# Kernel tuning notes

Hardware: AMD Instinct MI355X
Metric: run time of the kernel (lower is better)

Reference implementation:

```python
import jax, jax.numpy as jnp
import numpy as np

N = 50000      # nodes
E = 800000     # edges
IN = 128       # in_channels
HID = 32       # hidden_channels per head
HEADS = 4
OUT = 16       # out_channels
NEG_SLOPE_ATT = 0.2   # GATv2Conv default negative_slope
NEG_SLOPE_ACT = 0.01  # F.leaky_relu default
EPS = 1e-16


def setup_inputs() -> dict:
    key = jax.random.key(0)
    ks = jax.random.split(key, 13)
    d1 = HEADS * HID  # 128
    g = lambda k, shape, fan: jax.random.normal(k, shape, jnp.float32) * (1.0 / np.sqrt(fan))
    return {
        "x": jax.random.normal(ks[0], (N, IN), jnp.float32),
        "edge_index": jax.random.randint(ks[1], (2, E), 0, N, dtype=jnp.int32),
        "edge_weight": jax.random.uniform(ks[2], (E,), jnp.float32),
        # conv1 (GATv2): lin_l, lin_r, att, bias
        "Wl1": g(ks[3], (IN, d1), IN), "Wr1": g(ks[4], (IN, d1), IN),
        "att1": g(ks[5], (HEADS, HID), HID), "b1": jnp.zeros((d1,), jnp.float32),
        # conv2
        "Wl2": g(ks[6], (d1, d1), d1), "Wr2": g(ks[7], (d1, d1), d1),
        "att2": g(ks[8], (HEADS, HID), HID), "b2": jnp.zeros((d1,), jnp.float32),
        # classifier
        "Wc": g(ks[9], (d1, OUT), d1), "bc": jnp.zeros((OUT,), jnp.float32),
    }


def gatv2_layer(x, Wl, Wr, att, bias, src, dst):
    n = x.shape[0]
    xl = (x @ Wl).reshape(n, HEADS, HID)  # source transform
    xr = (x @ Wr).reshape(n, HEADS, HID)  # target transform
    m = xl[src] + xr[dst]                                    # [Etot, H, C]
    e = jnp.sum(jax.nn.leaky_relu(m, NEG_SLOPE_ATT) * att, axis=-1)  # [Etot, H]
    # segment softmax over incoming edges of each target node
    emax = jax.ops.segment_max(e, dst, num_segments=n)       # [N, H]
    ex = jnp.exp(e - emax[dst])
    denom = jax.ops.segment_sum(ex, dst, num_segments=n)     # [N, H]
    alpha = ex / (denom[dst] + EPS)                          # [Etot, H]
    out = jax.ops.segment_sum(xl[src] * alpha[:, :, None], dst, num_segments=n)  # [N, H, C]
    return out.reshape(n, HEADS * HID) + bias


def reference(x, edge_index, edge_weight, Wl1, Wr1, att1, b1, Wl2, Wr2, att2, b2, Wc, bc):
    # GATv2Conv default add_self_loops=True
    loops = jnp.arange(N, dtype=edge_index.dtype)
    src = jnp.concatenate([edge_index[0], loops])
    dst = jnp.concatenate([edge_index[1], loops])
    h = gatv2_layer(x, Wl1, Wr1, att1, b1, src, dst)
    h = jax.nn.leaky_relu(h, NEG_SLOPE_ACT)
    h = gatv2_layer(h, Wl2, Wr2, att2, b2, src, dst)
    h = jax.nn.leaky_relu(h, NEG_SLOPE_ACT)
    logits = h @ Wc + bc
    return (logits, h)
```

## Files before the change

### kernel.cpp

```cpp
#include <hip/hip_runtime.h>
#include <hip/hip_fp16.h>


#define LOG2E 1.4426950408889634f
#define AST 40

typedef short bf16x8 __attribute__((ext_vector_type(8)));
typedef float f32x4 __attribute__((ext_vector_type(4)));

__device__ __forceinline__ unsigned short f2bf(float f) {
  union { float f; unsigned u; } x; x.f = f;
  unsigned r = x.u + 0x7fffu + ((x.u >> 16) & 1u);
  return (unsigned short)(r >> 16);
}
__device__ __forceinline__ float bf2f(unsigned short h) {
  union { unsigned u; float f; } x; x.u = ((unsigned)h) << 16;
  return x.f;
}
__device__ __forceinline__ void split4(float4 v, ushort4& h, ushort4& l) {
  h.x = f2bf(v.x); l.x = f2bf(v.x - bf2f(h.x));
  h.y = f2bf(v.y); l.y = f2bf(v.y - bf2f(h.y));
  h.z = f2bf(v.z); l.z = f2bf(v.z - bf2f(h.z));
  h.w = f2bf(v.w); l.w = f2bf(v.w - bf2f(h.w));
}


__global__ __launch_bounds__(256) void zero_i32(int* __restrict__ p, int n) {
  int i = blockIdx.x * 256 + threadIdx.x;
  if (i < n) p[i] = 0;
}

__global__ __launch_bounds__(256) void count_kernel(const int* __restrict__ dst,
                                                    int* __restrict__ cnt, int E) {
  int i = blockIdx.x * 256 + threadIdx.x;
  if (i < E) atomicAdd(&cnt[dst[i]], 1);
}

__global__ __launch_bounds__(256) void scan_blk(const int* __restrict__ cnt,
                                                int* __restrict__ excl,
                                                int* __restrict__ bsum, int n) {
  __shared__ int s[256];
  int t = threadIdx.x, i = blockIdx.x * 256 + t;
  int v = (i < n) ? (cnt[i] + 1) : 0;
  s[t] = v;
  __syncthreads();
#pragma unroll
  for (int off = 1; off < 256; off <<= 1) {
    int u = (t >= off) ? s[t - off] : 0;
    __syncthreads();
    s[t] += u;
    __syncthreads();
  }
  if (i < n) excl[i] = s[t] - v;
  if (t == 255) bsum[blockIdx.x] = s[255];
}

__global__ __launch_bounds__(256) void scan_bsum(int* __restrict__ bsum, int nb,
                                                 int* __restrict__ row_start, int n) {
  __shared__ int s[256];
  int t = threadIdx.x;
  int v = (t < nb) ? bsum[t] : 0;
  s[t] = v;
  __syncthreads();
#pragma unroll
  for (int off = 1; off < 256; off <<= 1) {
    int u = (t >= off) ? s[t - off] : 0;
    __syncthreads();
    s[t] += u;
    __syncthreads();
  }
  if (t < nb) bsum[t] = s[t] - v;
  if (t == 255) row_start[n] = s[255];
}

__global__ __launch_bounds__(256) void scan_add(int* __restrict__ row_start,
                                                const int* __restrict__ bsum,
                                                int* __restrict__ wpos,
                                                int* __restrict__ csr,
                                                int n, int padBase) {
  int i = blockIdx.x * 256 + threadIdx.x;
  if (i < n) {
    int r = row_start[i] + bsum[blockIdx.x];
    row_start[i] = r;
    wpos[i] = r + 1;
    csr[r] = i;
  }
  if (blockIdx.x == 0 && threadIdx.x < 16) csr[padBase + threadIdx.x] = 0;
}

__global__ __launch_bounds__(256) void scatter_kernel(const int* __restrict__ src,
                                                      const int* __restrict__ dst,
                                                      int* __restrict__ wpos,
                                                      int* __restrict__ csr,
                                                      int E, int sliceSize) {
  int slice = blockIdx.x & 7;
  int chunk = blockIdx.x >> 3;
  int nchunk = gridDim.x >> 3;
  int lo = slice * sliceSize, hi = lo + sliceSize;
  int per = (E + nchunk - 1) / nchunk;
  int b = chunk * per;
  int e = min(b + per, E);
  for (int i = b + threadIdx.x; i < e; i += 256) {
    int d = dst[i];
    if (d >= lo && d < hi) {
      int p = atomicAdd(&wpos[d], 1);
      csr[p] = src[i];
    }
  }
}

__global__ __launch_bounds__(256) void convert_W(const float* __restrict__ Wl1,
                                                 const float* __restrict__ Wr1,
                                                 const float* __restrict__ Wl2,
                                                 const float* __restrict__ Wr2,
                                                 unsigned short* __restrict__ BT1h,
                                                 unsigned short* __restrict__ BT1l,
                                                 unsigned short* __restrict__ BT2h,
                                                 unsigned short* __restrict__ BT2l) {
  int b = blockIdx.x;
  const float* Wl = (b < 128) ? Wl1 : Wl2;
  const float* Wr = (b < 128) ? Wr1 : Wr2;
  unsigned short* BTh = (b < 128) ? BT1h : BT2h;
  unsigned short* BTl = (b < 128) ? BT1l : BT2l;
  int idx = (b & 127) * 256 + threadIdx.x;
  int col = idx >> 7, k = idx & 127;
  float v = (col < 128) ? Wl[k * 128 + col] : Wr[k * 128 + (col - 128)];
  unsigned short h = f2bf(v);
  BTh[idx] = h;
  BTl[idx] = f2bf(v - bf2f(h));
}

enum { IN_F32 = 0, IN_F16 = 1 };
template <int MODE>
__global__ __launch_bounds__(256) void gemm_mfma(
    const float* __restrict__ Af, const __half* __restrict__ Af16,
    const unsigned short* __restrict__ BTh, const unsigned short* __restrict__ BTl,
    __half* __restrict__ Cl, __half* __restrict__ Cr, int nrows) {
  __shared__ unsigned short sAh[128 * AST], sAl[128 * AST];
  __shared__ unsigned short sBh[128 * AST], sBl[128 * AST];
  int tid = threadIdx.x;
  int wave = tid >> 6, lane = tid & 63;
  int rowBase = blockIdx.x * 128;
  int colBase = blockIdx.y * 128;
  int rowHalf = (wave >> 1) * 64;
  int colHalf = (wave & 1) * 64;
  int l15 = lane & 15, quad = lane >> 4;

  f32x4 acc[4][4];
#pragma unroll
  for (int m = 0; m < 4; ++m)
#pragma unroll
    for (int n = 0; n < 4; ++n) acc[m][n] = (f32x4){0.f, 0.f, 0.f, 0.f};

  for (int kc = 0; kc < 4; ++kc) {
#pragma unroll
    for (int i = 0; i < 2; ++i) {
      int idx = tid + i * 256;
      int row = idx >> 2, seg = idx & 3;
      int gr = rowBase + row;
      if (MODE == IN_F32) {
        float4 v0 = make_float4(0.f, 0.f, 0.f, 0.f), v1 = v0;
        if (gr < nrows) {
          v0 = *(const float4*)&Af[(size_t)gr * 128 + kc * 32 + seg * 8];
          v1 = *(const float4*)&Af[(size_t)gr * 128 + kc * 32 + seg * 8 + 4];
        }
        ushort4 h0, l0, h1, l1;
        split4(v0, h0, l0);
        split4(v1, h1, l1);
        *(ushort4*)&sAh[row * AST + seg * 8] = h0;
        *(ushort4*)&sAh[row * AST + seg * 8 + 4] = h1;
        *(ushort4*)&sAl[row * AST + seg * 8] = l0;
        *(ushort4*)&sAl[row * AST + seg * 8 + 4] = l1;
      } else {
        uint4 raw = make_uint4(0, 0, 0, 0);
        if (gr < nrows)
          raw = *(const uint4*)&Af16[(size_t)gr * 128 + kc * 32 + seg * 8];
        const __half* hp = (const __half*)&raw;
        float4 v0 = make_float4(__half2float(hp[0]), __half2float(hp[1]),
                                __half2float(hp[2]), __half2float(hp[3]));
        float4 v1 = make_float4(__half2float(hp[4]), __half2float(hp[5]),
                                __half2float(hp[6]), __half2float(hp[7]));
        ushort4 h0, l0, h1, l1;
        split4(v0, h0, l0);
        split4(v1, h1, l1);
        *(ushort4*)&sAh[row * AST + seg * 8] = h0;
        *(ushort4*)&sAh[row * AST + seg * 8 + 4] = h1;
        *(ushort4*)&sAl[row * AST + seg * 8] = l0;
        *(ushort4*)&sAl[row * AST + seg * 8 + 4] = l1;
      }
    }
#pragma unroll
    for (int i = 0; i < 2; ++i) {
      int idx = tid + i * 256;
      int col = idx >> 2, seg = idx & 3;
      *(uint4*)&sBh[col * AST + seg * 8] =
          *(const uint4*)&BTh[(size_t)(colBase + col) * 128 + kc * 32 + seg * 8];
      *(uint4*)&sBl[col * AST + seg * 8] =
          *(const uint4*)&BTl[(size_t)(colBase + col) * 128 + kc * 32 + seg * 8];
    }
    __syncthreads();

    bf16x8 afh[4], afl[4], bfh[4], bfl[4];
#pragma unroll
    for (int m = 0; m < 4; ++m) {
      int r = rowHalf + m * 16 + l15;
      afh[m] = *(const bf16x8*)&sAh[r * AST + quad * 8];
      afl[m] = *(const bf16x8*)&sAl[r * AST + quad * 8];
    }
#pragma unroll
    for (int n = 0; n < 4; ++n) {
      int cc = colHalf + n * 16 + l15;
      bfh[n] = *(const bf16x8*)&sBh[cc * AST + quad * 8];
      bfl[n] = *(const bf16x8*)&sBl[cc * AST + quad * 8];
    }
#pragma unroll
    for (int m = 0; m < 4; ++m)
#pragma unroll
      for (int n = 0; n < 4; ++n) {
        acc[m][n] = __builtin_amdgcn_mfma_f32_16x16x32_bf16(afh[m], bfh[n], acc[m][n], 0, 0, 0);
        acc[m][n] = __builtin_amdgcn_mfma_f32_16x16x32_bf16(afh[m], bfl[n], acc[m][n], 0, 0, 0);
        acc[m][n] = __builtin_amdgcn_mfma_f32_16x16x32_bf16(afl[m], bfh[n], acc[m][n], 0, 0, 0);
      }
    __syncthreads();
  }

  __half* __restrict__ C = (blockIdx.y == 0) ? Cl : Cr;
#pragma unroll
  for (int m = 0; m < 4; ++m)
#pragma unroll
    for (int r = 0; r < 4; ++r) {
      int grow = rowBase + rowHalf + m * 16 + quad * 4 + r;
      if (grow < nrows) {
#pragma unroll
        for (int n = 0; n < 4; ++n)
          C[(size_t)grow * 128 + colHalf + n * 16 + l15] = __float2half(acc[m][n][r]);
      }
    }
}

__global__ __launch_bounds__(256) void gat_attn(const __half* __restrict__ xl,
                                                const __half* __restrict__ xr,
                                                const int* __restrict__ row_start,
                                                const int* __restrict__ csr,
                                                const float* __restrict__ att,
                                                const float* __restrict__ bias,
                                                float* __restrict__ ofp,
                                                __half* __restrict__ oh16,
                                                int n_nodes) {
  int node = blockIdx.x * 4 + (threadIdx.x >> 6);
  if (node >= n_nodes) return;
  int lane = threadIdx.x & 63;
  int slot = lane >> 4;
  int l15 = lane & 15;
  int c0 = l15 * 8;

  float fxr[8];
  {
    uint4 raw = *(const uint4*)&xr[(size_t)node * 128 + c0];
    const __half* hp = (const __half*)&raw;
#pragma unroll
    for (int k = 0; k < 8; ++k) fxr[k] = __half2float(hp[k]);
  }
  float a06[8], a04[8];
  {
    float4 a0 = *(const float4*)&att[c0];
    float4 a1 = *(const float4*)&att[c0 + 4];
    float av[8] = {a0.x, a0.y, a0.z, a0.w, a1.x, a1.y, a1.z, a1.w};
    const float C06 = 0.6f * LOG2E, C04 = 0.4f * LOG2E;
#pragma unroll
    for (int k = 0; k < 8; ++k) { a06[k] = av[k] * C06; a04[k] = av[k] * C04; }
  }

  float acc[8];
#pragma unroll
  for (int k = 0; k < 8; ++k) acc[k] = 0.f;
  float lsum = 0.f;

#define EDGE_BODY(SRC, PVALID)                                                 \
  {                                                                            \
    uint4 raw = *(const uint4*)&xl[(size_t)(unsigned)(SRC)*128 + c0];          \
    const __half* hp = (const __half*)&raw;                                    \
    float e = 0.f;                                                             \
    _Pragma("unroll") for (int k = 0; k < 8; ++k) {                            \
      float t = __half2float(hp[k]) + fxr[k];                                  \
      e = fmaf(a06[k], t, e);                                                  \
      e = fmaf(a04[k], fabsf(t), e);                                           \
    }                                                                          \
    e += __shfl_xor(e, 1);                                                     \
    e += __shfl_xor(e, 2);                                                     \
    float p = (PVALID) ? __builtin_amdgcn_exp2f(e) : 0.f;                      \
    lsum += p;                                                                 \
    _Pragma("unroll") for (int k = 0; k < 8; ++k)                              \
        acc[k] = fmaf(p, __half2float(hp[k]), acc[k]);                         \
  }

  int beg = row_start[node], end = row_start[node + 1];
  int deg = end - beg;
  int fullEnd = beg + (deg & ~15);

  for (int base = beg; base < fullEnd; base += 16) {
    int b0 = base + 4 * slot;
    int s0 = csr[b0], s1 = csr[b0 + 1], s2 = csr[b0 + 2], s3 = csr[b0 + 3];
    EDGE_BODY(s0, true);
    EDGE_BODY(s1, true);
    EDGE_BODY(s2, true);
    EDGE_BODY(s3, true);
  }
  for (int base = fullEnd; base < end; base += 4) {
    int idx = base + slot;
    int src = csr[idx];
    EDGE_BODY(src, idx < end);
  }
#undef EDGE_BODY

  lsum += __shfl_xor(lsum, 16);
  lsum += __shfl_xor(lsum, 32);
#pragma unroll
  for (int k = 0; k < 8; ++k) {
    acc[k] += __shfl_xor(acc[k], 16);
    acc[k] += __shfl_xor(acc[k], 32);
  }

  if (slot == 0) {
    float4 b0v = *(const float4*)&bias[c0];
    float4 b1v = *(const float4*)&bias[c0 + 4];
    float bv[8] = {b0v.x, b0v.y, b0v.z, b0v.w, b1v.x, b1v.y, b1v.z, b1v.w};
    float inv = 1.f / (lsum + 1e-16f);
    float o[8];
#pragma unroll
    for (int k = 0; k < 8; ++k) {
      float v = fmaf(acc[k], inv, bv[k]);
      o[k] = fmaf(0.495f, fabsf(v), 0.505f * v);
    }
    if (ofp) {
      *(float4*)&ofp[(size_t)node * 128 + c0] = make_float4(o[0], o[1], o[2], o[3]);
      *(float4*)&ofp[(size_t)node * 128 + c0 + 4] = make_float4(o[4], o[5], o[6], o[7]);
    }
    if (oh16) {
      ushort4 ha, hb;
      ha.x = __half_as_ushort(__float2half(o[0]));
      ha.y = __half_as_ushort(__float2half(o[1]));
      ha.z = __half_as_ushort(__float2half(o[2]));
      ha.w = __half_as_ushort(__float2half(o[3]));
      hb.x = __half_as_ushort(__float2half(o[4]));
      hb.y = __half_as_ushort(__float2half(o[5]));
      hb.z = __half_as_ushort(__float2half(o[6]));
      hb.w = __half_as_ushort(__float2half(o[7]));
      *(ushort4*)&oh16[(size_t)node * 128 + c0] = ha;
      *(ushort4*)&oh16[(size_t)node * 128 + c0 + 4] = hb;
    }
  }
}

__global__ __launch_bounds__(256) void classifier_kernel(const float4* __restrict__ h4,
                                                         const float* __restrict__ Wc,
                                                         const float* __restrict__ bc,
                                                         float* __restrict__ logits,
                                                         int n) {
  __shared__ float sW[2048];
  __shared__ float sb[16];
  int t = threadIdx.x;
#pragma unroll
  for (int i = 0; i < 8; ++i) sW[t + i * 256] = Wc[t + i * 256];
  if (t < 16) sb[t] = bc[t];
  __syncthreads();
  int node = blockIdx.x * 256 + t;
  if (node >= n) return;
  float acc[16];
#pragma unroll
  for (int o = 0; o < 16; ++o) acc[o] = sb[o];
  for (int c4 = 0; c4 < 32; ++c4) {
    float4 hv = h4[(unsigned)node * 32 + c4];
    const float* w = &sW[c4 * 64];
#pragma unroll
    for (int o = 0; o < 16; ++o) {
      acc[o] = fmaf(hv.x, w[o], acc[o]);
      acc[o] = fmaf(hv.y, w[16 + o], acc[o]);
      acc[o] = fmaf(hv.z, w[32 + o], acc[o]);
      acc[o] = fmaf(hv.w, w[48 + o], acc[o]);
    }
  }
#pragma unroll
  for (int q = 0; q < 4; ++q)
    *(float4*)&logits[(size_t)node * 16 + q * 4] =
        make_float4(acc[q * 4], acc[q * 4 + 1], acc[q * 4 + 2], acc[q * 4 + 3]);
}


extern "C" void kernel_launch(void* const* d_in, const int* in_sizes, int n_in,
                              void* d_out, int out_size, void* d_ws, size_t ws_size,
                              hipStream_t stream) {
  const float* x    = (const float*)d_in[0];
  const int*   ei   = (const int*)d_in[1];
  const float* Wl1  = (const float*)d_in[3];
  const float* Wr1  = (const float*)d_in[4];
  const float* att1 = (const float*)d_in[5];
  const float* b1   = (const float*)d_in[6];
  const float* Wl2  = (const float*)d_in[7];
  const float* Wr2  = (const float*)d_in[8];
  const float* att2 = (const float*)d_in[9];
  const float* b2   = (const float*)d_in[10];
  const float* Wc   = (const float*)d_in[11];
  const float* bc   = (const float*)d_in[12];

  const int N = in_sizes[0] / 128;
  const int E = in_sizes[1] / 2;

  float* outp   = (float*)d_out;
  float* logits = outp;
  float* hout   = outp + (size_t)N * 16;
  __half* h1f16 = (__half*)hout;

  char* ws = (char*)d_ws;
  __half* xlbuf = (__half*)ws;                ws += (size_t)N * 128 * 2;
  __half* xrbuf = (__half*)ws;                ws += (size_t)N * 128 * 2;
  unsigned short* WT1h = (unsigned short*)ws; ws += 256 * 128 * 2;
  unsigned short* WT1l = (unsigned short*)ws; ws += 256 * 128 * 2;
  unsigned short* WT2h = (unsigned short*)ws; ws += 256 * 128 * 2;
  unsigned short* WT2l = (unsigned short*)ws; ws += 256 * 128 * 2;
  int* cnt       = (int*)ws;                  ws += (size_t)N * 4;
  int* row_start = (int*)ws;                  ws += (size_t)(N + 1) * 4;
  int* wpos      = (int*)ws;                  ws += (size_t)N * 4;
  int* bsum      = (int*)ws;                  ws += 256 * 4;
  int* csr       = (int*)ws;                  ws += (size_t)(E + N + 16) * 4;

  const int* esrc = ei;
  const int* edst = ei + E;

  int gN = (N + 255) / 256, gE = (E + 255) / 256;
  dim3 gGemm((N + 127) / 128, 2);
  int gAttn = (N + 3) / 4;
  int sliceSize = (N + 7) / 8;

  zero_i32<<<gN, 256, 0, stream>>>(cnt, N);
  count_kernel<<<gE, 256, 0, stream>>>(edst, cnt, E);
  scan_blk<<<gN, 256, 0, stream>>>(cnt, row_start, bsum, N);
  scan_bsum<<<1, 256, 0, stream>>>(bsum, gN, row_start, N);
  scan_add<<<gN, 256, 0, stream>>>(row_start, bsum, wpos, csr, N, E + N);
  scatter_kernel<<<1024, 256, 0, stream>>>(esrc, edst, wpos, csr, E, sliceSize);

  convert_W<<<256, 256, 0, stream>>>(Wl1, Wr1, Wl2, Wr2, WT1h, WT1l, WT2h, WT2l);

  gemm_mfma<IN_F32><<<gGemm, 256, 0, stream>>>(x, nullptr, WT1h, WT1l,
                                               xlbuf, xrbuf, N);
  gat_attn<<<gAttn, 256, 0, stream>>>(xlbuf, xrbuf, row_start, csr, att1, b1,
                                      nullptr, h1f16, N);

  gemm_mfma<IN_F16><<<gGemm, 256, 0, stream>>>(nullptr, h1f16, WT2h, WT2l,
                                               xlbuf, xrbuf, N);
  gat_attn<<<gAttn, 256, 0, stream>>>(xlbuf, xrbuf, row_start, csr, att2, b2,
                                      hout, nullptr, N);

  classifier_kernel<<<(N + 255) / 256, 256, 0, stream>>>((const float4*)hout, Wc, bc,
                                                         logits, N);
}
```

Baseline: 323.3 us.

## Co-schedule CSR scatter with layer-1 GEMM and merge weight conversion into count

The weight conversion is folded into the edge-count kernel as extra blocks. The CSR scatter becomes part of the layer-1 GEMM launch: groups of nine blocks hold five scatter blocks and four GEMM tiles, so the atomic-bound scatter can overlap MFMA work. This removes two launches and their serialization. It also unrolls the scatter loop four times, reads esrc only for edges that fall in the block's slice, and raises wave priority around the MFMA section, at the cost of more complex block indexing and mixed resource usage in one grid.

```diff
diff --git a/kernel.cpp b/kernel.cpp
--- a/kernel.cpp
+++ b/kernel.cpp
@@ -28,12 +28,6 @@
 __global__ __launch_bounds__(256) void zero_i32(int* __restrict__ p, int n) {
   int i = blockIdx.x * 256 + threadIdx.x;
   if (i < n) p[i] = 0;
-}
-
-__global__ __launch_bounds__(256) void count_kernel(const int* __restrict__ dst,
-                                                    int* __restrict__ cnt, int E) {
-  int i = blockIdx.x * 256 + threadIdx.x;
-  if (i < E) atomicAdd(&cnt[dst[i]], 1);
 }
 
 __global__ __launch_bounds__(256) void scan_blk(const int* __restrict__ cnt,
@@ -88,36 +82,18 @@
   if (blockIdx.x == 0 && threadIdx.x < 16) csr[padBase + threadIdx.x] = 0;
 }
 
-__global__ __launch_bounds__(256) void scatter_kernel(const int* __restrict__ src,
-                                                      const int* __restrict__ dst,
-                                                      int* __restrict__ wpos,
-                                                      int* __restrict__ csr,
-                                                      int E, int sliceSize) {
-  int slice = blockIdx.x & 7;
-  int chunk = blockIdx.x >> 3;
-  int nchunk = gridDim.x >> 3;
-  int lo = slice * sliceSize, hi = lo + sliceSize;
-  int per = (E + nchunk - 1) / nchunk;
-  int b = chunk * per;
-  int e = min(b + per, E);
-  for (int i = b + threadIdx.x; i < e; i += 256) {
-    int d = dst[i];
-    if (d >= lo && d < hi) {
-      int p = atomicAdd(&wpos[d], 1);
-      csr[p] = src[i];
-    }
-  }
-}
-
-__global__ __launch_bounds__(256) void convert_W(const float* __restrict__ Wl1,
-                                                 const float* __restrict__ Wr1,
-                                                 const float* __restrict__ Wl2,
-                                                 const float* __restrict__ Wr2,
-                                                 unsigned short* __restrict__ BT1h,
-                                                 unsigned short* __restrict__ BT1l,
-                                                 unsigned short* __restrict__ BT2h,
-                                                 unsigned short* __restrict__ BT2l) {
+__global__ __launch_bounds__(256) void convert_count(
+    const float* __restrict__ Wl1, const float* __restrict__ Wr1,
+    const float* __restrict__ Wl2, const float* __restrict__ Wr2,
+    unsigned short* __restrict__ BT1h, unsigned short* __restrict__ BT1l,
+    unsigned short* __restrict__ BT2h, unsigned short* __restrict__ BT2l,
+    const int* __restrict__ dst, int* __restrict__ cnt, int E) {
   int b = blockIdx.x;
+  if (b >= 256) {
+    int i = (b - 256) * 256 + threadIdx.x;
+    if (i < E) atomicAdd(&cnt[dst[i]], 1);
+    return;
+  }
   const float* Wl = (b < 128) ? Wl1 : Wl2;
   const float* Wr = (b < 128) ? Wr1 : Wr2;
   unsigned short* BTh = (b < 128) ? BT1h : BT2h;
@@ -131,17 +107,84 @@
 }
 
 enum { IN_F32 = 0, IN_F16 = 1 };
-template <int MODE>
+#define NSCAT 1152
+#define NCHUNK 128
+template <int MODE, int FUSE>
 __global__ __launch_bounds__(256) void gemm_mfma(
     const float* __restrict__ Af, const __half* __restrict__ Af16,
     const unsigned short* __restrict__ BTh, const unsigned short* __restrict__ BTl,
-    __half* __restrict__ Cl, __half* __restrict__ Cr, int nrows) {
-  __shared__ unsigned short sAh[128 * AST], sAl[128 * AST];
-  __shared__ unsigned short sBh[128 * AST], sBl[128 * AST];
+    __half* __restrict__ Cl, __half* __restrict__ Cr, int nrows,
+    const int* __restrict__ esrc, const int* __restrict__ edst,
+    int* __restrict__ wpos, int* __restrict__ csr, int E, int sliceSize) {
+  __shared__ __align__(16) unsigned short smem[4 * 128 * AST];
   int tid = threadIdx.x;
+  int bx, by;
+  if (FUSE) {
+    int g = blockIdx.x / 9, r = blockIdx.x - g * 9;
+    if (r < 5) {
+      int sid = g * 5 + r;
+      if (sid < NSCAT) {
+        int slice = blockIdx.x & 7;
+        int chunk = (g >> 3) * 5;
+        for (int gp = g & ~7; gp < g; ++gp)
+          chunk += (((slice - gp) & 7) < 5) ? 1 : 0;
+        if (chunk < NCHUNK) {
+          int per = (E + NCHUNK - 1) / NCHUNK;
+          int b0 = chunk * per;
+          int ee = min(b0 + per, E);
+          int lo = slice * sliceSize, hi = lo + sliceSize;
+          int i = b0 + tid;
+          for (; i + 768 < ee; i += 1024) {
+            int d0 = edst[i];
+            int d1 = edst[i + 256];
+            int d2 = edst[i + 512];
+            int d3 = edst[i + 768];
+            if (d0 >= lo && d0 < hi) {
+              int s = esrc[i];
+              int p = atomicAdd(&wpos[d0], 1); csr[p] = s;
+            }
+            if (d1 >= lo && d1 < hi) {
+              int s = esrc[i + 256];
+              int p = atomicAdd(&wpos[d1], 1); csr[p] = s;
+            }
+            if (d2 >= lo && d2 < hi) {
+              int s = esrc[i + 512];
+              int p = atomicAdd(&wpos[d2], 1); csr[p] = s;
+            }
+            if (d3 >= lo && d3 < hi) {
+              int s = esrc[i + 768];
+              int p = atomicAdd(&wpos[d3], 1); csr[p] = s;
+            }
+          }
+          for (; i < ee; i += 256) {
+            int d = edst[i];
+            if (d >= lo && d < hi) {
+              int s = esrc[i];
+              int p = atomicAdd(&wpos[d], 1); csr[p] = s;
+            }
+          }
+        }
+      }
+      return;
+    }
+    int gid = g * 4 + (r - 5);
+    int nbx = (nrows + 127) >> 7;
+    if (gid >= nbx * 2) return;
+    bx = gid >> 1;
+    by = gid & 1;
+  } else {
+    bx = blockIdx.x;
+    by = blockIdx.y;
+  }
+
+  unsigned short* sAh = smem;
+  unsigned short* sAl = smem + 5120;
+  unsigned short* sBh = smem + 10240;
+  unsigned short* sBl = smem + 15360;
+
   int wave = tid >> 6, lane = tid & 63;
-  int rowBase = blockIdx.x * 128;
-  int colBase = blockIdx.y * 128;
+  int rowBase = bx * 128;
+  int colBase = by * 128;
   int rowHalf = (wave >> 1) * 64;
   int colHalf = (wave & 1) * 64;
   int l15 = lane & 15, quad = lane >> 4;
@@ -158,36 +201,29 @@
       int idx = tid + i * 256;
       int row = idx >> 2, seg = idx & 3;
       int gr = rowBase + row;
+      float4 v0 = make_float4(0.f, 0.f, 0.f, 0.f), v1 = v0;
       if (MODE == IN_F32) {
-        float4 v0 = make_float4(0.f, 0.f, 0.f, 0.f), v1 = v0;
         if (gr < nrows) {
           v0 = *(const float4*)&Af[(size_t)gr * 128 + kc * 32 + seg * 8];
           v1 = *(const float4*)&Af[(size_t)gr * 128 + kc * 32 + seg * 8 + 4];
         }
-        ushort4 h0, l0, h1, l1;
-        split4(v0, h0, l0);
-        split4(v1, h1, l1);
-        *(ushort4*)&sAh[row * AST + seg * 8] = h0;
-        *(ushort4*)&sAh[row * AST + seg * 8 + 4] = h1;
-        *(ushort4*)&sAl[row * AST + seg * 8] = l0;
-        *(ushort4*)&sAl[row * AST + seg * 8 + 4] = l1;
       } else {
-        uint4 raw = make_uint4(0, 0, 0, 0);
-        if (gr < nrows)
-          raw = *(const uint4*)&Af16[(size_t)gr * 128 + kc * 32 + seg * 8];
-        const __half* hp = (const __half*)&raw;
-        float4 v0 = make_float4(__half2float(hp[0]), __half2float(hp[1]),
-                                __half2float(hp[2]), __half2float(hp[3]));
-        float4 v1 = make_float4(__half2float(hp[4]), __half2float(hp[5]),
-                                __half2float(hp[6]), __half2float(hp[7]));
-        ushort4 h0, l0, h1, l1;
-        split4(v0, h0, l0);
-        split4(v1, h1, l1);
-        *(ushort4*)&sAh[row * AST + seg * 8] = h0;
-        *(ushort4*)&sAh[row * AST + seg * 8 + 4] = h1;
-        *(ushort4*)&sAl[row * AST + seg * 8] = l0;
-        *(ushort4*)&sAl[row * AST + seg * 8 + 4] = l1;
+        if (gr < nrows) {
+          uint4 raw = *(const uint4*)&Af16[(size_t)gr * 128 + kc * 32 + seg * 8];
+          const __half* hp = (const __half*)&raw;
+          v0 = make_float4(__half2float(hp[0]), __half2float(hp[1]),
+                           __half2float(hp[2]), __half2float(hp[3]));
+          v1 = make_float4(__half2float(hp[4]), __half2float(hp[5]),
+                           __half2float(hp[6]), __half2float(hp[7]));
+        }
       }
+      ushort4 h0, l0, h1, l1;
+      split4(v0, h0, l0);
+      split4(v1, h1, l1);
+      *(ushort4*)&sAh[row * AST + seg * 8] = h0;
+      *(ushort4*)&sAh[row * AST + seg * 8 + 4] = h1;
+      *(ushort4*)&sAl[row * AST + seg * 8] = l0;
+      *(ushort4*)&sAl[row * AST + seg * 8 + 4] = l1;
     }
 #pragma unroll
     for (int i = 0; i < 2; ++i) {
@@ -213,6 +249,7 @@
       bfh[n] = *(const bf16x8*)&sBh[cc * AST + quad * 8];
       bfl[n] = *(const bf16x8*)&sBl[cc * AST + quad * 8];
     }
+    __builtin_amdgcn_s_setprio(1);
 #pragma unroll
     for (int m = 0; m < 4; ++m)
 #pragma unroll
@@ -221,10 +258,11 @@
         acc[m][n] = __builtin_amdgcn_mfma_f32_16x16x32_bf16(afh[m], bfl[n], acc[m][n], 0, 0, 0);
         acc[m][n] = __builtin_amdgcn_mfma_f32_16x16x32_bf16(afl[m], bfh[n], acc[m][n], 0, 0, 0);
       }
+    __builtin_amdgcn_s_setprio(0);
     __syncthreads();
   }
 
-  __half* __restrict__ C = (blockIdx.y == 0) ? Cl : Cr;
+  __half* __restrict__ C = (by == 0) ? Cl : Cr;
 #pragma unroll
   for (int m = 0; m < 4; ++m)
 #pragma unroll
@@ -428,26 +466,33 @@
   const int* edst = ei + E;
 
   int gN = (N + 255) / 256, gE = (E + 255) / 256;
-  dim3 gGemm((N + 127) / 128, 2);
   int gAttn = (N + 3) / 4;
   int sliceSize = (N + 7) / 8;
 
+  int nbx = (N + 127) / 128;
+  int nGemm = nbx * 2;
+  int groups = (NSCAT + 4) / 5;
+  int g2 = (nGemm + 3) / 4;
+  if (g2 > groups) groups = g2;
+  int gFused = groups * 9;
+
   zero_i32<<<gN, 256, 0, stream>>>(cnt, N);
-  count_kernel<<<gE, 256, 0, stream>>>(edst, cnt, E);
+  convert_count<<<256 + gE, 256, 0, stream>>>(Wl1, Wr1, Wl2, Wr2,
+                                              WT1h, WT1l, WT2h, WT2l,
+                                              edst, cnt, E);
   scan_blk<<<gN, 256, 0, stream>>>(cnt, row_start, bsum, N);
   scan_bsum<<<1, 256, 0, stream>>>(bsum, gN, row_start, N);
   scan_add<<<gN, 256, 0, stream>>>(row_start, bsum, wpos, csr, N, E + N);
-  scatter_kernel<<<1024, 256, 0, stream>>>(esrc, edst, wpos, csr, E, sliceSize);
-
-  convert_W<<<256, 256, 0, stream>>>(Wl1, Wr1, Wl2, Wr2, WT1h, WT1l, WT2h, WT2l);
-
-  gemm_mfma<IN_F32><<<gGemm, 256, 0, stream>>>(x, nullptr, WT1h, WT1l,
-                                               xlbuf, xrbuf, N);
+
+  gemm_mfma<IN_F32, 1><<<gFused, 256, 0, stream>>>(
+      x, nullptr, WT1h, WT1l, xlbuf, xrbuf, N,
+      esrc, edst, wpos, csr, E, sliceSize);
   gat_attn<<<gAttn, 256, 0, stream>>>(xlbuf, xrbuf, row_start, csr, att1, b1,
                                       nullptr, h1f16, N);
 
-  gemm_mfma<IN_F16><<<gGemm, 256, 0, stream>>>(nullptr, h1f16, WT2h, WT2l,
-                                               xlbuf, xrbuf, N);
+  gemm_mfma<IN_F16, 0><<<dim3(nbx, 2), 256, 0, stream>>>(
+      nullptr, h1f16, WT2h, WT2l, xlbuf, xrbuf, N,
+      nullptr, nullptr, nullptr, nullptr, 0, 0);
   gat_attn<<<gAttn, 256, 0, stream>>>(xlbuf, xrbuf, row_start, csr, att2, b2,
                                       hout, nullptr, N);
 
```

Result: faster. 314.3 us (-2.8%).
